# Performance work log

Hardware: AMD Instinct MI355X
Metric: run time of the kernel (lower is better)

Reference implementation:

```python
import jax, jax.numpy as jnp
import numpy as np

N, D, V, T = 2048, 64, 32000, 512
K_WTA = 256
X_DECAY, U_DECAY = 0.97, 0.97
SPIKE_RATE = 0.01
FORGET_ETA = 0.01
HOMEO_TAU = 1.0
GAMMA_MAX = 1.0


def ln_row(z, eps=1e-6):
    # torch .std is unbiased (ddof=1)
    m = z.mean(-1, keepdims=True)
    s = z.std(-1, ddof=1, keepdims=True)
    return (z - m) / (s + eps)


def setup_inputs() -> dict:
    key = jax.random.key(0)
    ks = jax.random.split(key, 6)
    return {
        "tokens": jax.random.randint(ks[0], (T,), 0, V),
        "spike_u": jax.random.uniform(ks[1], (T, N), dtype=jnp.float32),
        "E": jax.random.normal(ks[2], (D, N), dtype=jnp.float32) / np.sqrt(N).astype(np.float32),
        "Dx": jax.random.normal(ks[3], (N, D), dtype=jnp.float32) / np.sqrt(D).astype(np.float32),
        "Dy": jax.random.normal(ks[4], (N, D), dtype=jnp.float32) / np.sqrt(D).astype(np.float32),
        "token_emb": jax.random.normal(ks[5], (V, D), dtype=jnp.float32) / np.sqrt(D).astype(np.float32),
    }


def reference(tokens, spike_u, E, Dx, Dy, token_emb):
    def step(carry, inp):
        x, rho = carry
        tok, u = inp
        v_prev = token_emb[tok]                                   # (D,)
        x_t = X_DECAY * x + jax.nn.relu(Dx @ v_prev)              # (N,)
        x_t = x_t / (jnp.sum(jnp.abs(x_t)) + 1e-6)                # L1 normalize
        a_hat = ln_row(rho @ x_t)                                 # (D,) ln_before_Dy
        # branches=4 with elementwise softplus == softplus on full matvec
        y_core = jax.nn.softplus(Dy @ a_hat)                      # (N,)
        y_core = y_core + (u < SPIKE_RATE).astype(y_core.dtype)   # spike noise
        # k-WTA: keep top K_WTA entries
        _, idx = jax.lax.top_k(y_core, K_WTA)
        mask = jnp.zeros((N,), bool).at[idx].set(True)
        y_core = y_core * mask.astype(y_core.dtype)
        y_t = jax.nn.relu(y_core) * jax.nn.relu(x_t)
        # homeostasis (torch uses .item() -> constant scale)
        s = y_t.sum()
        scale = jnp.where(s > 1e-8, jnp.minimum(1.0, HOMEO_TAU / (s + 1e-8)), 1.0)
        y_t = y_t * jax.lax.stop_gradient(scale)
        v_star = ln_row(E @ y_t)                                  # (D,)
        # surprisal gain (torch uses .item() -> constant)
        p = jax.nn.softmax(v_star)
        H = -(p * jnp.log(p + 1e-12)).sum()
        gain = jnp.minimum(GAMMA_MAX, H / jnp.log(jnp.float32(D) + 1e-6) * GAMMA_MAX)
        gain = jax.lax.stop_gradient(gain)
        # dynamic top-k on x_t via rank masking (jit-safe data-dependent k)
        k_dyn = jnp.clip((N * (0.05 + 0.25 * gain)).astype(jnp.int32), 1, N)
        order = jnp.argsort(-x_t)
        ranks = jnp.zeros((N,), jnp.int32).at[order].set(jnp.arange(N, dtype=jnp.int32))
        x_t = x_t * (ranks < k_dyn).astype(x_t.dtype)
        # local forgetting on inactive columns, then Hebbian update
        inactive = (x_t <= 0).astype(rho.dtype)
        rho = rho * (1.0 - FORGET_ETA * inactive[None, :])
        rho = U_DECAY * (rho + gain * jnp.outer(v_prev, x_t))
        return (x_t, rho), v_star

    init = (jnp.zeros((N,), jnp.float32), jnp.zeros((D, N), jnp.float32))
    (_, _), v_stack = jax.lax.scan(step, init, (tokens, spike_u))
    return v_stack  # (T, D)
```

## Files before the change

kernel.cpp:

```cpp
#include <hip/hip_runtime.h>
#include <math.h>

#define NB   16
#define NTH  256
#define CH   128
#define NN   2048
#define DD   64
#define TT   512
#define KWTA 256
#define PA   65
#define PB   132

struct __align__(128) BarFlag { unsigned v; unsigned pad[31]; };
__device__ BarFlag g_flag[NB];
__device__ __align__(16) float  g_rf[NB][DD];
__device__ __align__(16) double g_L1[NB];
__device__ __align__(16) float  g_xg[NN];
__device__ __align__(16) float  g_yg[NN];
__device__ __align__(16) float  g_ET[NN*DD];

__global__ void bdh_init(const float* __restrict__ E) {
  const int gid = blockIdx.x * NTH + threadIdx.x;
  if (gid < NB) g_flag[gid].v = 0u;
  for (int idx = gid; idx < NN * DD; idx += 64 * NTH) {
    const int n = idx >> 6, d = idx & 63;
    g_ET[idx] = E[(size_t)d * NN + n];
  }
}

__device__ __forceinline__ void grid_barrier(unsigned& epoch) {
  epoch += 1u;
  __syncthreads();
  if (threadIdx.x < 64) {
    if (threadIdx.x == 0) {
      __threadfence();
      __hip_atomic_store(&g_flag[blockIdx.x].v, epoch, __ATOMIC_RELAXED,
                         __HIP_MEMORY_SCOPE_AGENT);
    }
    const int i = (int)threadIdx.x;
    for (;;) {
      const bool ok = (i >= NB) ||
        (__hip_atomic_load(&g_flag[i].v, __ATOMIC_RELAXED,
                           __HIP_MEMORY_SCOPE_AGENT) >= epoch);
      if (__all(ok)) break;
      __builtin_amdgcn_s_sleep(1);
    }
    __builtin_amdgcn_fence(__ATOMIC_ACQUIRE, "agent");
  }
  __syncthreads();
}

__device__ __forceinline__ double wredd(double v) {
  #pragma unroll
  for (int off = 32; off > 0; off >>= 1) v += __shfl_xor(v, off, 64);
  return v;
}
__device__ __forceinline__ float wredf(float v) {
  #pragma unroll
  for (int off = 32; off > 0; off >>= 1) v += __shfl_xor(v, off, 64);
  return v;
}

__device__ __forceinline__ unsigned select_mask(const unsigned* __restrict__ keys,
                                                int K, int tid,
                                                unsigned* __restrict__ hist,
                                                unsigned* __restrict__ hist2,
                                                unsigned* __restrict__ cw)
{
  const int wv = tid >> 6, lane = tid & 63;
  const int sub = tid & 7;
  uint4* H4 = (uint4*)hist;
  const uint4 z4 = {0u, 0u, 0u, 0u};
  unsigned prefix = 0u, pmask = 0u;
  int remK = K;
  #pragma unroll
  for (int lev = 0; lev < 4; ++lev) {
    const int shf = 24 - 8 * lev;
    #pragma unroll
    for (int j = 0; j < 8; ++j)
      if ((keys[j] & pmask) == prefix)
        atomicAdd(&hist[(((keys[j] >> shf) & 255u) << 3) + sub], 1u);
    __syncthreads();
    {
      const uint4 a = H4[tid * 2], bq = H4[tid * 2 + 1];
      hist2[tid] = a.x + a.y + a.z + a.w + bq.x + bq.y + bq.z + bq.w;
      H4[tid * 2] = z4;
      H4[tid * 2 + 1] = z4;
    }
    __syncthreads();
    const uint4 cc = ((const uint4*)hist2)[lane];
    unsigned c[4] = {cc.x, cc.y, cc.z, cc.w};
    unsigned s[4];
    s[3] = c[3]; s[2] = c[2] + s[3]; s[1] = c[1] + s[2]; s[0] = c[0] + s[1];
    unsigned SS = s[0];
    #pragma unroll
    for (int off = 1; off < 64; off <<= 1) {
      const unsigned o = __shfl_down(SS, off, 64);
      if (lane + off < 64) SS += o;
    }
    const unsigned T = SS - s[0];
    unsigned pk = 0u;
    #pragma unroll
    for (int k = 0; k < 4; ++k) {
      const unsigned A = s[k] + T;
      if (A >= (unsigned)remK && (A - c[k]) < (unsigned)remK)
        pk = (((unsigned)(4 * lane + k)) << 16) | (unsigned)(remK - (int)(A - c[k]));
    }
    const unsigned long long bal = __ballot(pk != 0u);
    const int src = __ffsll((long long)bal) - 1;
    pk = __shfl(pk, src, 64);
    prefix |= (pk >> 16) << shf;
    remK = (int)(pk & 0xffffu);
    pmask |= 255u << shf;
  }
  const unsigned thr = prefix;
  const unsigned R = (unsigned)remK;
  unsigned lc[8], cnt = 0u;
  #pragma unroll
  for (int j = 0; j < 8; ++j) { lc[j] = cnt; cnt += (keys[j] == thr) ? 1u : 0u; }
  unsigned e = cnt;
  #pragma unroll
  for (int off = 1; off < 64; off <<= 1) {
    const unsigned o = __shfl_up(e, off, 64);
    if (lane >= off) e += o;
  }
  if (lane == 63) cw[wv] = e;
  __syncthreads();
  unsigned base = 0u;
  for (int w = 0; w < wv; ++w) base += cw[w];
  const unsigned excl = base + e - cnt;
  unsigned mask = 0u;
  #pragma unroll
  for (int j = 0; j < 8; ++j)
    if (keys[j] > thr || (keys[j] == thr && excl + lc[j] < R)) mask |= 1u << j;
  return mask;
}

__global__ void __launch_bounds__(NTH)
bdh_main(const int* __restrict__ tokens, const float* __restrict__ spike_u,
         const float* __restrict__ Emat, const float* __restrict__ Dx,
         const float* __restrict__ Dy, const float* __restrict__ temb,
         float* __restrict__ out)
{
  __shared__ float sh_rho[DD][PB];
  __shared__ float sh_Dx[CH][PA];
  __shared__ float sh_Dy[CH][PA];
  __shared__ int   sh_tok[TT];
  __shared__ float sh_v[2][DD];
  __shared__ float sh_xstate[CH];
  __shared__ float sh_xtun[CH];
  __shared__ float sh_ahat[DD];
  __shared__ float sh_ffac[CH];
  __shared__ unsigned sh_hist[256*8];
  __shared__ unsigned sh_hist2[256];
  __shared__ unsigned sh_cw[8];
  __shared__ float sh_fmisc[4];
  __shared__ double sh_dred[8];
  __shared__ double sh_rd[4][DD];
  __shared__ float sh_gred[4][DD];
  __shared__ int   sh_aidx[KWTA];
  __shared__ float sh_aw[KWTA];

  const int tid  = threadIdx.x;
  const int b    = blockIdx.x;
  const int n0   = b * CH;
  const int i2   = tid >> 1;
  const int p2   = tid & 1;
  const int d4   = tid >> 2;
  const int p4   = tid & 3;
  const int lane = tid & 63;
  const int wv   = tid >> 6;
  unsigned epoch = 0u;

  for (int k = tid; k < TT; k += NTH) sh_tok[k] = tokens[k];
  for (int k = tid; k < DD*PB; k += NTH) (&sh_rho[0][0])[k] = 0.0f;
  for (int k = tid; k < 256*8; k += NTH) sh_hist[k] = 0u;
  if (tid < CH) sh_xstate[tid] = 0.0f;
  for (int r = wv; r < CH; r += 4) {
    sh_Dx[r][lane] = Dx[(size_t)(n0 + r)*DD + lane];
    sh_Dy[r][lane] = Dy[(size_t)(n0 + r)*DD + lane];
  }
  __syncthreads();
  if (tid < DD) sh_v[0][tid] = temb[(size_t)sh_tok[0]*DD + tid];
  __syncthreads();

  for (int t = 0; t < TT; ++t) {
    const int par = t & 1;

    float spu = 0.0f;
    if (p2 == 0) spu = spike_u[(size_t)t*NN + n0 + i2];
    if (t + 1 < TT && tid < DD)
      sh_v[par ^ 1][tid] = temb[(size_t)sh_tok[t + 1]*DD + tid];

    float d1 = 0.0f;
    {
      const float* dxr = &sh_Dx[i2][p2*32];
      const float* vv  = &sh_v[par][p2*32];
      #pragma unroll
      for (int j = 0; j < 32; ++j) d1 += dxr[j] * vv[j];
    }
    d1 += __shfl_xor(d1, 1, 64);
    float xnew = 0.0f;
    if (p2 == 0) {
      xnew = 0.97f * sh_xstate[i2] + fmaxf(d1, 0.0f);
      sh_xtun[i2] = xnew;
    }
    {
      double v = (p2 == 0) ? (double)fabsf(xnew) : 0.0;
      v = wredd(v);
      if (lane == 0) sh_dred[wv] = v;
      __syncthreads();
      if (tid == 0) g_L1[b] = sh_dred[0] + sh_dred[1] + sh_dred[2] + sh_dred[3];
    }
    float qa = 0.0f;
    {
      const float* rr = &sh_rho[d4][0];
      #pragma unroll
      for (int j = 0; j < 32; ++j) { const int c = p4 + 4*j; qa += rr[c] * sh_xtun[c]; }
    }
    qa += __shfl_xor(qa, 1, 64);
    qa += __shfl_xor(qa, 2, 64);
    if (p4 == 0) g_rf[b][d4] = qa;
    grid_barrier(epoch);

    {
      double acc = 0.0;
      #pragma unroll
      for (int j = 0; j < 4; ++j) acc += (double)g_rf[(wv<<2) + j][lane];
      sh_rd[wv][lane] = acc;
    }
    if (tid < 64) {
      double v = (tid < NB) ? g_L1[tid] : 0.0;
      v = wredd(v);
      if (tid == 0) sh_dred[0] = v;
    }
    __syncthreads();
    const float Lden = (float)sh_dred[0] + 1e-6f;
    if (tid < 64) {
      const double qd = sh_rd[0][tid] + sh_rd[1][tid] + sh_rd[2][tid] + sh_rd[3][tid];
      const float rf = (float)qd / Lden;
      const float m  = wredf(rf) * (1.0f/64.0f);
      const float dv = rf - m;
      const float sd = sqrtf(wredf(dv*dv) * (1.0f/63.0f));
      sh_ahat[tid] = dv / (sd + 1e-6f);
    } else if (tid < 192) {
      const int l = tid - 64;
      g_xg[n0 + l] = sh_xtun[l] / Lden;
    }
    __syncthreads();
    float d2 = 0.0f;
    {
      const float* dyr = &sh_Dy[i2][p2*32];
      const float* aa  = &sh_ahat[p2*32];
      #pragma unroll
      for (int j = 0; j < 32; ++j) d2 += dyr[j] * aa[j];
    }
    d2 += __shfl_xor(d2, 1, 64);
    if (p2 == 0) {
      const float sp = fmaxf(d2, 0.0f) + log1pf(expf(-fabsf(d2)));
      g_yg[n0 + i2] = sp + ((spu < 0.01f) ? 1.0f : 0.0f);
    }
    grid_barrier(epoch);

    unsigned ykeys[8], xkeys[8];
    {
      const float4* py = ((const float4*)g_yg) + tid*2;
      const float4* px = ((const float4*)g_xg) + tid*2;
      const float4 y0 = py[0], y1 = py[1];
      const float4 x0 = px[0], x1 = px[1];
      ykeys[0]=__float_as_uint(y0.x); ykeys[1]=__float_as_uint(y0.y);
      ykeys[2]=__float_as_uint(y0.z); ykeys[3]=__float_as_uint(y0.w);
      ykeys[4]=__float_as_uint(y1.x); ykeys[5]=__float_as_uint(y1.y);
      ykeys[6]=__float_as_uint(y1.z); ykeys[7]=__float_as_uint(y1.w);
      xkeys[0]=__float_as_uint(x0.x); xkeys[1]=__float_as_uint(x0.y);
      xkeys[2]=__float_as_uint(x0.z); xkeys[3]=__float_as_uint(x0.w);
      xkeys[4]=__float_as_uint(x1.x); xkeys[5]=__float_as_uint(x1.y);
      xkeys[6]=__float_as_uint(x1.z); xkeys[7]=__float_as_uint(x1.w);
    }
    const unsigned km = select_mask(ykeys, KWTA, tid, sh_hist, sh_hist2, sh_cw);
    float p[8]; unsigned nzm = 0u;
    #pragma unroll
    for (int j = 0; j < 8; ++j) {
      const float yv = __uint_as_float(ykeys[j]);
      const float xv = __uint_as_float(xkeys[j]);
      p[j] = yv * xv;
      if (((km >> j) & 1u) && xv > 0.0f) nzm |= 1u << j;
    }
    const unsigned cnt = (unsigned)__popc(nzm);
    {
      double sp = 0.0;
      #pragma unroll
      for (int j = 0; j < 8; ++j) if ((nzm >> j) & 1u) sp += (double)p[j];
      sp = wredd(sp);
      if (lane == 0) sh_dred[wv] = sp;
    }
    unsigned e = cnt;
    #pragma unroll
    for (int off = 1; off < 64; off <<= 1) {
      const unsigned o = __shfl_up(e, off, 64);
      if (lane >= off) e += o;
    }
    if (lane == 63) sh_cw[4 + wv] = e;
    __syncthreads();
    const float sf = (float)(sh_dred[0] + sh_dred[1] + sh_dred[2] + sh_dred[3]);
    const float scale = (sf > 1e-8f) ? fminf(1.0f, 1.0f/(sf + 1e-8f)) : 1.0f;
    const int m = (int)(sh_cw[4] + sh_cw[5] + sh_cw[6] + sh_cw[7]);
    {
      unsigned base = 0u;
      for (int w = 0; w < wv; ++w) base += sh_cw[4 + w];
      int pos = (int)(base + e - cnt);
      #pragma unroll
      for (int j = 0; j < 8; ++j)
        if ((nzm >> j) & 1u) { sh_aidx[pos] = 8*tid + j; sh_aw[pos] = scale * p[j]; ++pos; }
    }
    __syncthreads();
    {
      float a0 = 0.0f, a1 = 0.0f, a2 = 0.0f, a3 = 0.0f;
      int i = wv;
      for (; i + 12 < m; i += 16) {
        a0 = fmaf(sh_aw[i],      g_ET[(size_t)sh_aidx[i]     *DD + lane], a0);
        a1 = fmaf(sh_aw[i + 4],  g_ET[(size_t)sh_aidx[i + 4] *DD + lane], a1);
        a2 = fmaf(sh_aw[i + 8],  g_ET[(size_t)sh_aidx[i + 8] *DD + lane], a2);
        a3 = fmaf(sh_aw[i + 12], g_ET[(size_t)sh_aidx[i + 12]*DD + lane], a3);
      }
      for (; i < m; i += 4)
        a0 = fmaf(sh_aw[i], g_ET[(size_t)sh_aidx[i]*DD + lane], a0);
      sh_gred[wv][lane] = (a0 + a1) + (a2 + a3);
    }
    __syncthreads();
    if (tid < 64) {
      const float z = sh_gred[0][tid] + sh_gred[1][tid] + sh_gred[2][tid] + sh_gred[3][tid];
      const float mn = wredf(z) * (1.0f/64.0f);
      const float dv = z - mn;
      const float sd = sqrtf(wredf(dv*dv) * (1.0f/63.0f));
      const float vs = dv / (sd + 1e-6f);
      if (b == 0) out[t*DD + tid] = vs;
      float mx = vs;
      #pragma unroll
      for (int off = 32; off > 0; off >>= 1) mx = fmaxf(mx, __shfl_xor(mx, off, 64));
      const float ex = expf(vs - mx);
      const float se = wredf(ex);
      const float pp = ex / se;
      const float ht = wredf(-pp * logf(pp + 1e-12f));
      if (tid == 0) sh_fmisc[0] = fminf(1.0f, ht / logf(64.0f));
    }
    __syncthreads();
    const float gain = sh_fmisc[0];
    int kd = (int)(2048.0f * (0.05f + 0.25f * gain));
    kd = kd < 1 ? 1 : (kd > NN ? NN : kd);
    const unsigned xm = select_mask(xkeys, kd, tid, sh_hist, sh_hist2, sh_cw);
    #pragma unroll
    for (int j = 0; j < 8; ++j) {
      const int g = 8*tid + j;
      const unsigned l = (unsigned)(g - n0);
      if (l < (unsigned)CH) {
        const float xv = __uint_as_float(xkeys[j]);
        const float v = ((xm >> j) & 1u) ? xv : 0.0f;
        sh_xstate[l] = v;
        sh_ffac[l] = (v <= 0.0f) ? (1.0f - 0.01f) : 1.0f;
      }
    }
    __syncthreads();
    {
      const float vd = sh_v[par][d4];
      float* rr = &sh_rho[d4][0];
      #pragma unroll
      for (int j = 0; j < 32; ++j) {
        const int c = p4 + 4*j;
        rr[c] = 0.97f * (rr[c]*sh_ffac[c] + gain * (vd * sh_xstate[c]));
      }
    }
    __syncthreads();
  }
}

extern "C" void kernel_launch(void* const* d_in, const int* in_sizes, int n_in,
                              void* d_out, int out_size, void* d_ws, size_t ws_size,
                              hipStream_t stream) {
  const int*   tokens = (const int*)d_in[0];
  const float* spike  = (const float*)d_in[1];
  const float* Emat   = (const float*)d_in[2];
  const float* Dx     = (const float*)d_in[3];
  const float* Dy     = (const float*)d_in[4];
  const float* temb   = (const float*)d_in[5];
  float* out = (float*)d_out;
  (void)in_sizes; (void)n_in; (void)out_size; (void)d_ws; (void)ws_size;
  bdh_init<<<dim3(64), dim3(NTH), 0, stream>>>(Emat);
  bdh_main<<<dim3(NB), dim3(NTH), 0, stream>>>(tokens, spike, Emat, Dx, Dy, temb, out);
}
```

Before: 9.981 ms.

## Switch top-k selection to 12/12/8-bit radix passes and split grid barrier

Measured after the change: 10.07 ms. Within noise of the previous version (+0.9%).

```diff
diff --git a/kernel.cpp b/kernel.cpp
--- a/kernel.cpp
+++ b/kernel.cpp
@@ -28,15 +28,17 @@
   }
 }
 
-__device__ __forceinline__ void grid_barrier(unsigned& epoch) {
+__device__ __forceinline__ void bar_arrive(unsigned& epoch) {
   epoch += 1u;
   __syncthreads();
+  if (threadIdx.x == 0) {
+    __threadfence();
+    __hip_atomic_store(&g_flag[blockIdx.x].v, epoch, __ATOMIC_RELAXED,
+                       __HIP_MEMORY_SCOPE_AGENT);
+  }
+}
+__device__ __forceinline__ void bar_wait(unsigned epoch) {
   if (threadIdx.x < 64) {
-    if (threadIdx.x == 0) {
-      __threadfence();
-      __hip_atomic_store(&g_flag[blockIdx.x].v, epoch, __ATOMIC_RELAXED,
-                         __HIP_MEMORY_SCOPE_AGENT);
-    }
     const int i = (int)threadIdx.x;
     for (;;) {
       const bool ok = (i >= NB) ||
@@ -61,60 +63,85 @@
   return v;
 }
 
-__device__ __forceinline__ unsigned select_mask(const unsigned* __restrict__ keys,
-                                                int K, int tid,
-                                                unsigned* __restrict__ hist,
-                                                unsigned* __restrict__ hist2,
-                                                unsigned* __restrict__ cw)
-{
+__device__ __forceinline__ uint2 scan4096(const unsigned* __restrict__ h,
+                                          unsigned* __restrict__ coarse,
+                                          int tid, int lane, unsigned remK) {
+  const uint4* H4 = (const uint4*)h;
+  unsigned tot = 0u;
+  #pragma unroll
+  for (int k = 0; k < 4; ++k) {
+    const uint4 q = H4[tid * 4 + k];
+    tot += q.x + q.y + q.z + q.w;
+  }
+  coarse[tid] = tot;
+  __syncthreads();
+  const uint4 C = ((const uint4*)coarse)[lane];
+  const unsigned s3 = C.w, s2 = C.z + s3, s1 = C.y + s2, s0 = C.x + s1;
+  unsigned SS = s0;
+  #pragma unroll
+  for (int off = 1; off < 64; off <<= 1) {
+    const unsigned o = __shfl_down(SS, off, 64);
+    if (lane + off < 64) SS += o;
+  }
+  const unsigned T = SS - s0;
+  const unsigned cs[4] = {C.x, C.y, C.z, C.w};
+  const unsigned sf[4] = {s0, s1, s2, s3};
+  unsigned pk = 0u;
+  #pragma unroll
+  for (int k = 0; k < 4; ++k) {
+    const unsigned A = sf[k] + T;
+    if (A >= remK && A - cs[k] < remK)
+      pk = (((unsigned)(4 * lane + k)) << 16) | (remK - (A - cs[k]));
+  }
+  const unsigned long long bal = __ballot(pk != 0u);
+  const int src = __ffsll((long long)bal) - 1;
+  pk = __shfl(pk, src, 64);
+  const int tc = (int)(pk >> 16);
+  const unsigned rk = pk & 0xffffu;
+  const uint4 f0 = H4[tc*4+0], f1 = H4[tc*4+1], f2 = H4[tc*4+2], f3 = H4[tc*4+3];
+  const unsigned f[16] = {f0.x,f0.y,f0.z,f0.w, f1.x,f1.y,f1.z,f1.w,
+                          f2.x,f2.y,f2.z,f2.w, f3.x,f3.y,f3.z,f3.w};
+  unsigned FS[16];
+  FS[15] = f[15];
+  #pragma unroll
+  for (int k = 14; k >= 0; --k) FS[k] = f[k] + FS[k + 1];
+  unsigned bin = 0u, rem = rk;
+  #pragma unroll
+  for (int k = 0; k < 16; ++k)
+    if (FS[k] >= rk && FS[k] - f[k] < rk) { bin = (unsigned)(16*tc + k); rem = rk - (FS[k] - f[k]); }
+  return make_uint2(bin, rem);
+}
+
+__device__ __forceinline__ uint2 scan256(const unsigned* __restrict__ h,
+                                         int lane, unsigned remK) {
+  const uint4 C = ((const uint4*)h)[lane];
+  const unsigned s3 = C.w, s2 = C.z + s3, s1 = C.y + s2, s0 = C.x + s1;
+  unsigned SS = s0;
+  #pragma unroll
+  for (int off = 1; off < 64; off <<= 1) {
+    const unsigned o = __shfl_down(SS, off, 64);
+    if (lane + off < 64) SS += o;
+  }
+  const unsigned T = SS - s0;
+  const unsigned cs[4] = {C.x, C.y, C.z, C.w};
+  const unsigned sf[4] = {s0, s1, s2, s3};
+  unsigned pk = 0u;
+  #pragma unroll
+  for (int k = 0; k < 4; ++k) {
+    const unsigned A = sf[k] + T;
+    if (A >= remK && A - cs[k] < remK)
+      pk = (((unsigned)(4 * lane + k)) << 16) | (remK - (A - cs[k]));
+  }
+  const unsigned long long bal = __ballot(pk != 0u);
+  const int src = __ffsll((long long)bal) - 1;
+  pk = __shfl(pk, src, 64);
+  return make_uint2(pk >> 16, pk & 0xffffu);
+}
+
+__device__ __forceinline__ unsigned tie_mask(const unsigned* __restrict__ keys,
+                                             unsigned thr, unsigned R, int tid,
+                                             unsigned* __restrict__ cw) {
   const int wv = tid >> 6, lane = tid & 63;
-  const int sub = tid & 7;
-  uint4* H4 = (uint4*)hist;
-  const uint4 z4 = {0u, 0u, 0u, 0u};
-  unsigned prefix = 0u, pmask = 0u;
-  int remK = K;
-  #pragma unroll
-  for (int lev = 0; lev < 4; ++lev) {
-    const int shf = 24 - 8 * lev;
-    #pragma unroll
-    for (int j = 0; j < 8; ++j)
-      if ((keys[j] & pmask) == prefix)
-        atomicAdd(&hist[(((keys[j] >> shf) & 255u) << 3) + sub], 1u);
-    __syncthreads();
-    {
-      const uint4 a = H4[tid * 2], bq = H4[tid * 2 + 1];
-      hist2[tid] = a.x + a.y + a.z + a.w + bq.x + bq.y + bq.z + bq.w;
-      H4[tid * 2] = z4;
-      H4[tid * 2 + 1] = z4;
-    }
-    __syncthreads();
-    const uint4 cc = ((const uint4*)hist2)[lane];
-    unsigned c[4] = {cc.x, cc.y, cc.z, cc.w};
-    unsigned s[4];
-    s[3] = c[3]; s[2] = c[2] + s[3]; s[1] = c[1] + s[2]; s[0] = c[0] + s[1];
-    unsigned SS = s[0];
-    #pragma unroll
-    for (int off = 1; off < 64; off <<= 1) {
-      const unsigned o = __shfl_down(SS, off, 64);
-      if (lane + off < 64) SS += o;
-    }
-    const unsigned T = SS - s[0];
-    unsigned pk = 0u;
-    #pragma unroll
-    for (int k = 0; k < 4; ++k) {
-      const unsigned A = s[k] + T;
-      if (A >= (unsigned)remK && (A - c[k]) < (unsigned)remK)
-        pk = (((unsigned)(4 * lane + k)) << 16) | (unsigned)(remK - (int)(A - c[k]));
-    }
-    const unsigned long long bal = __ballot(pk != 0u);
-    const int src = __ffsll((long long)bal) - 1;
-    pk = __shfl(pk, src, 64);
-    prefix |= (pk >> 16) << shf;
-    remK = (int)(pk & 0xffffu);
-    pmask |= 255u << shf;
-  }
-  const unsigned thr = prefix;
-  const unsigned R = (unsigned)remK;
   unsigned lc[8], cnt = 0u;
   #pragma unroll
   for (int j = 0; j < 8; ++j) { lc[j] = cnt; cnt += (keys[j] == thr) ? 1u : 0u; }
@@ -151,8 +178,10 @@
   __shared__ float sh_xtun[CH];
   __shared__ float sh_ahat[DD];
   __shared__ float sh_ffac[CH];
-  __shared__ unsigned sh_hist[256*8];
-  __shared__ unsigned sh_hist2[256];
+  __shared__ __align__(16) unsigned sh_h1x[4096];
+  __shared__ __align__(16) unsigned sh_h1y[4096];
+  __shared__ __align__(16) unsigned sh_h3[256];
+  __shared__ __align__(16) unsigned sh_coarse[256];
   __shared__ unsigned sh_cw[8];
   __shared__ float sh_fmisc[4];
   __shared__ double sh_dred[8];
@@ -171,10 +200,16 @@
   const int lane = tid & 63;
   const int wv   = tid >> 6;
   unsigned epoch = 0u;
+  const uint4 z4 = {0u, 0u, 0u, 0u};
 
   for (int k = tid; k < TT; k += NTH) sh_tok[k] = tokens[k];
   for (int k = tid; k < DD*PB; k += NTH) (&sh_rho[0][0])[k] = 0.0f;
-  for (int k = tid; k < 256*8; k += NTH) sh_hist[k] = 0u;
+  {
+    uint4* Zx = (uint4*)sh_h1x; uint4* Zy = (uint4*)sh_h1y;
+    #pragma unroll
+    for (int k = 0; k < 4; ++k) { Zx[tid*4+k] = z4; Zy[tid*4+k] = z4; }
+    if (tid < 64) ((uint4*)sh_h3)[tid] = z4;
+  }
   if (tid < CH) sh_xstate[tid] = 0.0f;
   for (int r = wv; r < CH; r += 4) {
     sh_Dx[r][lane] = Dx[(size_t)(n0 + r)*DD + lane];
@@ -204,6 +239,7 @@
     if (p2 == 0) {
       xnew = 0.97f * sh_xstate[i2] + fmaxf(d1, 0.0f);
       sh_xtun[i2] = xnew;
+      g_xg[n0 + i2] = xnew;
     }
     {
       double v = (p2 == 0) ? (double)fabsf(xnew) : 0.0;
@@ -221,8 +257,11 @@
     qa += __shfl_xor(qa, 1, 64);
     qa += __shfl_xor(qa, 2, 64);
     if (p4 == 0) g_rf[b][d4] = qa;
-    grid_barrier(epoch);
-
+    bar_arrive(epoch);
+    bar_wait(epoch);
+
+    const float4* pxu = ((const float4*)g_xg) + tid*2;
+    const float4 xu0 = pxu[0], xu1 = pxu[1];
     {
       double acc = 0.0;
       #pragma unroll
@@ -239,13 +278,16 @@
     if (tid < 64) {
       const double qd = sh_rd[0][tid] + sh_rd[1][tid] + sh_rd[2][tid] + sh_rd[3][tid];
       const float rf = (float)qd / Lden;
-      const float m  = wredf(rf) * (1.0f/64.0f);
-      const float dv = rf - m;
+      const float mm = wredf(rf) * (1.0f/64.0f);
+      const float dv = rf - mm;
       const float sd = sqrtf(wredf(dv*dv) * (1.0f/63.0f));
       sh_ahat[tid] = dv / (sd + 1e-6f);
-    } else if (tid < 192) {
-      const int l = tid - 64;
-      g_xg[n0 + l] = sh_xtun[l] / Lden;
+    }
+    unsigned xkeys[8];
+    {
+      const float xf[8] = {xu0.x,xu0.y,xu0.z,xu0.w, xu1.x,xu1.y,xu1.z,xu1.w};
+      #pragma unroll
+      for (int j = 0; j < 8; ++j) xkeys[j] = __float_as_uint(xf[j] / Lden);
     }
     __syncthreads();
     float d2 = 0.0f;
@@ -260,24 +302,52 @@
       const float sp = fmaxf(d2, 0.0f) + log1pf(expf(-fabsf(d2)));
       g_yg[n0 + i2] = sp + ((spu < 0.01f) ? 1.0f : 0.0f);
     }
-    grid_barrier(epoch);
-
-    unsigned ykeys[8], xkeys[8];
+    bar_arrive(epoch);
+    #pragma unroll
+    for (int j = 0; j < 8; ++j) atomicAdd(&sh_h1x[xkeys[j] >> 20], 1u);
+    bar_wait(epoch);
+
+    unsigned ykeys[8];
     {
       const float4* py = ((const float4*)g_yg) + tid*2;
-      const float4* px = ((const float4*)g_xg) + tid*2;
       const float4 y0 = py[0], y1 = py[1];
-      const float4 x0 = px[0], x1 = px[1];
       ykeys[0]=__float_as_uint(y0.x); ykeys[1]=__float_as_uint(y0.y);
       ykeys[2]=__float_as_uint(y0.z); ykeys[3]=__float_as_uint(y0.w);
       ykeys[4]=__float_as_uint(y1.x); ykeys[5]=__float_as_uint(y1.y);
       ykeys[6]=__float_as_uint(y1.z); ykeys[7]=__float_as_uint(y1.w);
-      xkeys[0]=__float_as_uint(x0.x); xkeys[1]=__float_as_uint(x0.y);
-      xkeys[2]=__float_as_uint(x0.z); xkeys[3]=__float_as_uint(x0.w);
-      xkeys[4]=__float_as_uint(x1.x); xkeys[5]=__float_as_uint(x1.y);
-      xkeys[6]=__float_as_uint(x1.z); xkeys[7]=__float_as_uint(x1.w);
-    }
-    const unsigned km = select_mask(ykeys, KWTA, tid, sh_hist, sh_hist2, sh_cw);
+    }
+    #pragma unroll
+    for (int j = 0; j < 8; ++j) atomicAdd(&sh_h1y[ykeys[j] >> 20], 1u);
+    __syncthreads();
+    const uint2 yr1 = scan4096(sh_h1y, sh_coarse, tid, lane, KWTA);
+    __syncthreads();
+    {
+      uint4* Z = (uint4*)sh_h1y;
+      #pragma unroll
+      for (int k = 0; k < 4; ++k) Z[tid*4+k] = z4;
+    }
+    __syncthreads();
+    #pragma unroll
+    for (int j = 0; j < 8; ++j)
+      if ((ykeys[j] >> 20) == yr1.x)
+        atomicAdd(&sh_h1y[(ykeys[j] >> 8) & 4095u], 1u);
+    __syncthreads();
+    const uint2 yr2 = scan4096(sh_h1y, sh_coarse, tid, lane, yr1.y);
+    const unsigned ypre = (yr1.x << 12) | yr2.x;
+    #pragma unroll
+    for (int j = 0; j < 8; ++j)
+      if ((ykeys[j] >> 8) == ypre)
+        atomicAdd(&sh_h3[ykeys[j] & 255u], 1u);
+    __syncthreads();
+    const uint2 yr3 = scan256(sh_h3, lane, yr2.y);
+    const unsigned thrY = (ypre << 8) | yr3.x;
+    const unsigned km = tie_mask(ykeys, thrY, yr3.y, tid, sh_cw);
+    {
+      uint4* Z = (uint4*)sh_h1y;
+      #pragma unroll
+      for (int k = 0; k < 4; ++k) Z[tid*4+k] = z4;
+      if (tid < 64) ((uint4*)sh_h3)[tid] = z4;
+    }
     float p[8]; unsigned nzm = 0u;
     #pragma unroll
     for (int j = 0; j < 8; ++j) {
@@ -346,9 +416,35 @@
     }
     __syncthreads();
     const float gain = sh_fmisc[0];
-    int kd = (int)(2048.0f * (0.05f + 0.25f * gain));
-    kd = kd < 1 ? 1 : (kd > NN ? NN : kd);
-    const unsigned xm = select_mask(xkeys, kd, tid, sh_hist, sh_hist2, sh_cw);
+    int kdi = (int)(2048.0f * (0.05f + 0.25f * gain));
+    kdi = kdi < 1 ? 1 : (kdi > NN ? NN : kdi);
+    const uint2 xr1 = scan4096(sh_h1x, sh_coarse, tid, lane, (unsigned)kdi);
+    #pragma unroll
+    for (int j = 0; j < 8; ++j)
+      if ((xkeys[j] >> 20) == xr1.x)
+        atomicAdd(&sh_h1y[(xkeys[j] >> 8) & 4095u], 1u);
+    __syncthreads();
+    {
+      uint4* Z = (uint4*)sh_h1x;
+      #pragma unroll
+      for (int k = 0; k < 4; ++k) Z[tid*4+k] = z4;
+    }
+    const uint2 xr2 = scan4096(sh_h1y, sh_coarse, tid, lane, xr1.y);
+    const unsigned xpre = (xr1.x << 12) | xr2.x;
+    #pragma unroll
+    for (int j = 0; j < 8; ++j)
+      if ((xkeys[j] >> 8) == xpre)
+        atomicAdd(&sh_h3[xkeys[j] & 255u], 1u);
+    __syncthreads();
+    {
+      uint4* Z = (uint4*)sh_h1y;
+      #pragma unroll
+      for (int k = 0; k < 4; ++k) Z[tid*4+k] = z4;
+    }
+    const uint2 xr3 = scan256(sh_h3, lane, xr2.y);
+    const unsigned thrX = (xpre << 8) | xr3.x;
+    const unsigned xm = tie_mask(xkeys, thrX, xr3.y, tid, sh_cw);
+    if (tid < 64) ((uint4*)sh_h3)[tid] = z4;
     #pragma unroll
     for (int j = 0; j < 8; ++j) {
       const int g = 8*tid + j;
```

## Use cache-bypassing stores/loads to drop barrier fences and early-publish x

Applied to the files above, without the earlier changes.

Result: faster. 9.760 ms (-2.2%).

```diff
diff --git a/kernel.cpp b/kernel.cpp
--- a/kernel.cpp
+++ b/kernel.cpp
@@ -11,6 +11,8 @@
 #define PA   65
 #define PB   132
 
+typedef float f32x4 __attribute__((ext_vector_type(4)));
+
 struct __align__(128) BarFlag { unsigned v; unsigned pad[31]; };
 __device__ BarFlag g_flag[NB];
 __device__ __align__(16) float  g_rf[NB][DD];
@@ -28,15 +30,23 @@
   }
 }
 
-__device__ __forceinline__ void grid_barrier(unsigned& epoch) {
+__device__ __forceinline__ void st_coh_f32(float* p, float v) {
+  asm volatile("global_store_dword %0, %1, off sc0 sc1" :: "v"(p), "v"(v) : "memory");
+}
+__device__ __forceinline__ void st_coh_f64(double* p, double v) {
+  asm volatile("global_store_dwordx2 %0, %1, off sc0 sc1" :: "v"(p), "v"(v) : "memory");
+}
+
+__device__ __forceinline__ void bar_arrive(unsigned& epoch) {
   epoch += 1u;
+  asm volatile("s_waitcnt vmcnt(0)" ::: "memory");
   __syncthreads();
+  if (threadIdx.x == 0)
+    __hip_atomic_store(&g_flag[blockIdx.x].v, epoch, __ATOMIC_RELAXED,
+                       __HIP_MEMORY_SCOPE_AGENT);
+}
+__device__ __forceinline__ void bar_wait(unsigned epoch) {
   if (threadIdx.x < 64) {
-    if (threadIdx.x == 0) {
-      __threadfence();
-      __hip_atomic_store(&g_flag[blockIdx.x].v, epoch, __ATOMIC_RELAXED,
-                         __HIP_MEMORY_SCOPE_AGENT);
-    }
     const int i = (int)threadIdx.x;
     for (;;) {
       const bool ok = (i >= NB) ||
@@ -45,7 +55,6 @@
       if (__all(ok)) break;
       __builtin_amdgcn_s_sleep(1);
     }
-    __builtin_amdgcn_fence(__ATOMIC_ACQUIRE, "agent");
   }
   __syncthreads();
 }
@@ -204,13 +213,15 @@
     if (p2 == 0) {
       xnew = 0.97f * sh_xstate[i2] + fmaxf(d1, 0.0f);
       sh_xtun[i2] = xnew;
+      st_coh_f32(&g_xg[n0 + i2], xnew);
     }
     {
       double v = (p2 == 0) ? (double)fabsf(xnew) : 0.0;
       v = wredd(v);
       if (lane == 0) sh_dred[wv] = v;
       __syncthreads();
-      if (tid == 0) g_L1[b] = sh_dred[0] + sh_dred[1] + sh_dred[2] + sh_dred[3];
+      if (tid == 0) st_coh_f64(&g_L1[b],
+                               sh_dred[0] + sh_dred[1] + sh_dred[2] + sh_dred[3]);
     }
     float qa = 0.0f;
     {
@@ -220,18 +231,40 @@
     }
     qa += __shfl_xor(qa, 1, 64);
     qa += __shfl_xor(qa, 2, 64);
-    if (p4 == 0) g_rf[b][d4] = qa;
-    grid_barrier(epoch);
-
+    if (p4 == 0) st_coh_f32(&g_rf[b][d4], qa);
+    bar_arrive(epoch);
+    bar_wait(epoch);
+
+    f32x4 xu0, xu1; float rf0, rf1, rf2, rf3;
+    {
+      const float* xp = g_xg + tid*8;
+      const float* rp = &g_rf[wv*4][lane];
+      asm volatile(
+        "global_load_dwordx4 %0, %6, off sc0 sc1\n\t"
+        "global_load_dwordx4 %1, %6, off offset:16 sc0 sc1\n\t"
+        "global_load_dword %2, %7, off sc0 sc1\n\t"
+        "global_load_dword %3, %7, off offset:256 sc0 sc1\n\t"
+        "global_load_dword %4, %7, off offset:512 sc0 sc1\n\t"
+        "global_load_dword %5, %7, off offset:768 sc0 sc1\n\t"
+        "s_waitcnt vmcnt(0)"
+        : "=&v"(xu0), "=&v"(xu1), "=&v"(rf0), "=&v"(rf1), "=&v"(rf2), "=&v"(rf3)
+        : "v"(xp), "v"(rp)
+        : "memory");
+      __builtin_amdgcn_sched_barrier(0);
+    }
     {
       double acc = 0.0;
-      #pragma unroll
-      for (int j = 0; j < 4; ++j) acc += (double)g_rf[(wv<<2) + j][lane];
+      acc += (double)rf0; acc += (double)rf1; acc += (double)rf2; acc += (double)rf3;
       sh_rd[wv][lane] = acc;
     }
     if (tid < 64) {
-      double v = (tid < NB) ? g_L1[tid] : 0.0;
-      v = wredd(v);
+      double lv = 0.0;
+      if (tid < NB) {
+        asm volatile("global_load_dwordx2 %0, %1, off sc0 sc1\n\ts_waitcnt vmcnt(0)"
+                     : "=&v"(lv) : "v"(&g_L1[tid]) : "memory");
+      }
+      __builtin_amdgcn_sched_barrier(0);
+      const double v = wredd(lv);
       if (tid == 0) sh_dred[0] = v;
     }
     __syncthreads();
@@ -239,13 +272,16 @@
     if (tid < 64) {
       const double qd = sh_rd[0][tid] + sh_rd[1][tid] + sh_rd[2][tid] + sh_rd[3][tid];
       const float rf = (float)qd / Lden;
-      const float m  = wredf(rf) * (1.0f/64.0f);
-      const float dv = rf - m;
+      const float mm = wredf(rf) * (1.0f/64.0f);
+      const float dv = rf - mm;
       const float sd = sqrtf(wredf(dv*dv) * (1.0f/63.0f));
       sh_ahat[tid] = dv / (sd + 1e-6f);
-    } else if (tid < 192) {
-      const int l = tid - 64;
-      g_xg[n0 + l] = sh_xtun[l] / Lden;
+    }
+    unsigned xkeys[8];
+    {
+      const float xf[8] = {xu0[0],xu0[1],xu0[2],xu0[3], xu1[0],xu1[1],xu1[2],xu1[3]};
+      #pragma unroll
+      for (int j = 0; j < 8; ++j) xkeys[j] = __float_as_uint(xf[j] / Lden);
     }
     __syncthreads();
     float d2 = 0.0f;
@@ -258,24 +294,25 @@
     d2 += __shfl_xor(d2, 1, 64);
     if (p2 == 0) {
       const float sp = fmaxf(d2, 0.0f) + log1pf(expf(-fabsf(d2)));
-      g_yg[n0 + i2] = sp + ((spu < 0.01f) ? 1.0f : 0.0f);
-    }
-    grid_barrier(epoch);
-
-    unsigned ykeys[8], xkeys[8];
-    {
-      const float4* py = ((const float4*)g_yg) + tid*2;
-      const float4* px = ((const float4*)g_xg) + tid*2;
-      const float4 y0 = py[0], y1 = py[1];
-      const float4 x0 = px[0], x1 = px[1];
-      ykeys[0]=__float_as_uint(y0.x); ykeys[1]=__float_as_uint(y0.y);
-      ykeys[2]=__float_as_uint(y0.z); ykeys[3]=__float_as_uint(y0.w);
-      ykeys[4]=__float_as_uint(y1.x); ykeys[5]=__float_as_uint(y1.y);
-      ykeys[6]=__float_as_uint(y1.z); ykeys[7]=__float_as_uint(y1.w);
-      xkeys[0]=__float_as_uint(x0.x); xkeys[1]=__float_as_uint(x0.y);
-      xkeys[2]=__float_as_uint(x0.z); xkeys[3]=__float_as_uint(x0.w);
-      xkeys[4]=__float_as_uint(x1.x); xkeys[5]=__float_as_uint(x1.y);
-      xkeys[6]=__float_as_uint(x1.z); xkeys[7]=__float_as_uint(x1.w);
+      st_coh_f32(&g_yg[n0 + i2], sp + ((spu < 0.01f) ? 1.0f : 0.0f));
+    }
+    bar_arrive(epoch);
+    bar_wait(epoch);
+
+    unsigned ykeys[8];
+    {
+      f32x4 yv0, yv1;
+      const float* yp = g_yg + tid*8;
+      asm volatile(
+        "global_load_dwordx4 %0, %2, off sc0 sc1\n\t"
+        "global_load_dwordx4 %1, %2, off offset:16 sc0 sc1\n\t"
+        "s_waitcnt vmcnt(0)"
+        : "=&v"(yv0), "=&v"(yv1) : "v"(yp) : "memory");
+      __builtin_amdgcn_sched_barrier(0);
+      ykeys[0]=__float_as_uint(yv0[0]); ykeys[1]=__float_as_uint(yv0[1]);
+      ykeys[2]=__float_as_uint(yv0[2]); ykeys[3]=__float_as_uint(yv0[3]);
+      ykeys[4]=__float_as_uint(yv1[0]); ykeys[5]=__float_as_uint(yv1[1]);
+      ykeys[6]=__float_as_uint(yv1[2]); ykeys[7]=__float_as_uint(yv1[3]);
     }
     const unsigned km = select_mask(ykeys, KWTA, tid, sh_hist, sh_hist2, sh_cw);
     float p[8]; unsigned nzm = 0u;
@@ -346,9 +383,9 @@
     }
     __syncthreads();
     const float gain = sh_fmisc[0];
-    int kd = (int)(2048.0f * (0.05f + 0.25f * gain));
-    kd = kd < 1 ? 1 : (kd > NN ? NN : kd);
-    const unsigned xm = select_mask(xkeys, kd, tid, sh_hist, sh_hist2, sh_cw);
+    int kdi = (int)(2048.0f * (0.05f + 0.25f * gain));
+    kdi = kdi < 1 ? 1 : (kdi > NN ? NN : kdi);
+    const unsigned xm = select_mask(xkeys, kdi, tid, sh_hist, sh_hist2, sh_cw);
     #pragma unroll
     for (int j = 0; j < 8; ++j) {
       const int g = 8*tid + j;
```

## Replace grid barriers with tagged value-flag pairs polled by consumers

Applied to the files above, without the earlier changes.

After: 12.74 ms. 1.28x slower.

```diff
diff --git a/kernel.cpp b/kernel.cpp
--- a/kernel.cpp
+++ b/kernel.cpp
@@ -11,43 +11,32 @@
 #define PA   65
 #define PB   132
 
-struct __align__(128) BarFlag { unsigned v; unsigned pad[31]; };
-__device__ BarFlag g_flag[NB];
-__device__ __align__(16) float  g_rf[NB][DD];
-__device__ __align__(16) double g_L1[NB];
-__device__ __align__(16) float  g_xg[NN];
-__device__ __align__(16) float  g_yg[NN];
-__device__ __align__(16) float  g_ET[NN*DD];
+typedef unsigned long long u64;
+
+__device__ __align__(16) u64 g_xp[2][NN];
+__device__ __align__(16) u64 g_rp[2][NB][DD];
+__device__ __align__(16) u64 g_lp[2][NB][2];
+__device__ __align__(16) u64 g_yp[2][NN];
+__device__ __align__(16) float g_ET[NN*DD];
 
 __global__ void bdh_init(const float* __restrict__ E) {
   const int gid = blockIdx.x * NTH + threadIdx.x;
-  if (gid < NB) g_flag[gid].v = 0u;
-  for (int idx = gid; idx < NN * DD; idx += 64 * NTH) {
+  const int nthread = 64 * NTH;
+  for (int k = gid; k < 2*NN; k += nthread) { ((u64*)g_xp)[k] = 0ull; ((u64*)g_yp)[k] = 0ull; }
+  for (int k = gid; k < 2*NB*DD; k += nthread) ((u64*)g_rp)[k] = 0ull;
+  if (gid < 2*NB*2) ((u64*)g_lp)[gid] = 0ull;
+  for (int idx = gid; idx < NN * DD; idx += nthread) {
     const int n = idx >> 6, d = idx & 63;
     g_ET[idx] = E[(size_t)d * NN + n];
   }
 }
 
-__device__ __forceinline__ void grid_barrier(unsigned& epoch) {
-  epoch += 1u;
-  __syncthreads();
-  if (threadIdx.x < 64) {
-    if (threadIdx.x == 0) {
-      __threadfence();
-      __hip_atomic_store(&g_flag[blockIdx.x].v, epoch, __ATOMIC_RELAXED,
-                         __HIP_MEMORY_SCOPE_AGENT);
-    }
-    const int i = (int)threadIdx.x;
-    for (;;) {
-      const bool ok = (i >= NB) ||
-        (__hip_atomic_load(&g_flag[i].v, __ATOMIC_RELAXED,
-                           __HIP_MEMORY_SCOPE_AGENT) >= epoch);
-      if (__all(ok)) break;
-      __builtin_amdgcn_s_sleep(1);
-    }
-    __builtin_amdgcn_fence(__ATOMIC_ACQUIRE, "agent");
-  }
-  __syncthreads();
+__device__ __forceinline__ void st_pair(u64* p, unsigned valbits, unsigned tag) {
+  __hip_atomic_store(p, ((u64)tag << 32) | (u64)valbits,
+                     __ATOMIC_RELAXED, __HIP_MEMORY_SCOPE_AGENT);
+}
+__device__ __forceinline__ u64 ld_pair(const u64* p) {
+  return __hip_atomic_load(p, __ATOMIC_RELAXED, __HIP_MEMORY_SCOPE_AGENT);
 }
 
 __device__ __forceinline__ double wredd(double v) {
@@ -59,6 +48,19 @@
   #pragma unroll
   for (int off = 32; off > 0; off >>= 1) v += __shfl_xor(v, off, 64);
   return v;
+}
+
+__device__ __forceinline__ void poll8(const u64* __restrict__ p, unsigned want,
+                                      unsigned* __restrict__ outb) {
+  unsigned got = 0u;
+  while (got != 0xffu) {
+    #pragma unroll
+    for (int j = 0; j < 8; ++j)
+      if (!((got >> j) & 1u)) {
+        const u64 w = ld_pair(&p[j]);
+        if ((unsigned)(w >> 32) == want) { outb[j] = (unsigned)w; got |= 1u << j; }
+      }
+  }
 }
 
 __device__ __forceinline__ unsigned select_mask(const unsigned* __restrict__ keys,
@@ -156,7 +158,6 @@
   __shared__ unsigned sh_cw[8];
   __shared__ float sh_fmisc[4];
   __shared__ double sh_dred[8];
-  __shared__ double sh_rd[4][DD];
   __shared__ float sh_gred[4][DD];
   __shared__ int   sh_aidx[KWTA];
   __shared__ float sh_aw[KWTA];
@@ -170,7 +171,6 @@
   const int p4   = tid & 3;
   const int lane = tid & 63;
   const int wv   = tid >> 6;
-  unsigned epoch = 0u;
 
   for (int k = tid; k < TT; k += NTH) sh_tok[k] = tokens[k];
   for (int k = tid; k < DD*PB; k += NTH) (&sh_rho[0][0])[k] = 0.0f;
@@ -186,6 +186,7 @@
 
   for (int t = 0; t < TT; ++t) {
     const int par = t & 1;
+    const unsigned want = (unsigned)(t + 1);
 
     float spu = 0.0f;
     if (p2 == 0) spu = spike_u[(size_t)t*NN + n0 + i2];
@@ -204,13 +205,19 @@
     if (p2 == 0) {
       xnew = 0.97f * sh_xstate[i2] + fmaxf(d1, 0.0f);
       sh_xtun[i2] = xnew;
+      st_pair(&g_xp[par][n0 + i2], __float_as_uint(xnew), want);
     }
     {
       double v = (p2 == 0) ? (double)fabsf(xnew) : 0.0;
       v = wredd(v);
       if (lane == 0) sh_dred[wv] = v;
       __syncthreads();
-      if (tid == 0) g_L1[b] = sh_dred[0] + sh_dred[1] + sh_dred[2] + sh_dred[3];
+      if (tid == 0) {
+        const double L = sh_dred[0] + sh_dred[1] + sh_dred[2] + sh_dred[3];
+        const u64 lb = __double_as_longlong(L);
+        st_pair(&g_lp[par][b][0], (unsigned)lb, want);
+        st_pair(&g_lp[par][b][1], (unsigned)(lb >> 32), want);
+      }
     }
     float qa = 0.0f;
     {
@@ -220,32 +227,53 @@
     }
     qa += __shfl_xor(qa, 1, 64);
     qa += __shfl_xor(qa, 2, 64);
-    if (p4 == 0) g_rf[b][d4] = qa;
-    grid_barrier(epoch);
-
-    {
-      double acc = 0.0;
-      #pragma unroll
-      for (int j = 0; j < 4; ++j) acc += (double)g_rf[(wv<<2) + j][lane];
-      sh_rd[wv][lane] = acc;
-    }
-    if (tid < 64) {
-      double v = (tid < NB) ? g_L1[tid] : 0.0;
-      v = wredd(v);
-      if (tid == 0) sh_dred[0] = v;
-    }
-    __syncthreads();
-    const float Lden = (float)sh_dred[0] + 1e-6f;
-    if (tid < 64) {
-      const double qd = sh_rd[0][tid] + sh_rd[1][tid] + sh_rd[2][tid] + sh_rd[3][tid];
+    if (p4 == 0) st_pair(&g_rp[par][b][d4], __float_as_uint(qa), want);
+
+    double lv = 0.0;
+    if (lane < 16) {
+      unsigned got = 0u, lo = 0u, hi = 0u;
+      while (got != 3u) {
+        if (!(got & 1u)) { const u64 w = ld_pair(&g_lp[par][lane][0]);
+          if ((unsigned)(w >> 32) == want) { lo = (unsigned)w; got |= 1u; } }
+        if (!(got & 2u)) { const u64 w = ld_pair(&g_lp[par][lane][1]);
+          if ((unsigned)(w >> 32) == want) { hi = (unsigned)w; got |= 2u; } }
+      }
+      lv = __longlong_as_double(((u64)hi << 32) | (u64)lo);
+    }
+    const double L1tot = wredd(lv);
+    const float Lden = (float)L1tot + 1e-6f;
+    unsigned xub[8];
+    poll8(&g_xp[par][tid*8], want, xub);
+    unsigned xkeys[8];
+    #pragma unroll
+    for (int j = 0; j < 8; ++j)
+      xkeys[j] = __float_as_uint(__uint_as_float(xub[j]) / Lden);
+    if (wv == 0) {
+      float rv[16];
+      unsigned got = 0u;
+      while (got != 0xffffu) {
+        #pragma unroll
+        for (int bb = 0; bb < 16; ++bb)
+          if (!((got >> bb) & 1u)) {
+            const u64 w = ld_pair(&g_rp[par][bb][lane]);
+            if ((unsigned)(w >> 32) == want) { rv[bb] = __uint_as_float((unsigned)w); got |= 1u << bb; }
+          }
+      }
+      double a0 = 0.0, a1 = 0.0, a2 = 0.0, a3 = 0.0;
+      #pragma unroll
+      for (int j = 0; j < 4; ++j) a0 += (double)rv[j];
+      #pragma unroll
+      for (int j = 4; j < 8; ++j) a1 += (double)rv[j];
+      #pragma unroll
+      for (int j = 8; j < 12; ++j) a2 += (double)rv[j];
+      #pragma unroll
+      for (int j = 12; j < 16; ++j) a3 += (double)rv[j];
+      const double qd = ((a0 + a1) + a2) + a3;
       const float rf = (float)qd / Lden;
-      const float m  = wredf(rf) * (1.0f/64.0f);
-      const float dv = rf - m;
+      const float mm = wredf(rf) * (1.0f/64.0f);
+      const float dv = rf - mm;
       const float sd = sqrtf(wredf(dv*dv) * (1.0f/63.0f));
-      sh_ahat[tid] = dv / (sd + 1e-6f);
-    } else if (tid < 192) {
-      const int l = tid - 64;
-      g_xg[n0 + l] = sh_xtun[l] / Lden;
+      sh_ahat[lane] = dv / (sd + 1e-6f);
     }
     __syncthreads();
     float d2 = 0.0f;
@@ -258,25 +286,12 @@
     d2 += __shfl_xor(d2, 1, 64);
     if (p2 == 0) {
       const float sp = fmaxf(d2, 0.0f) + log1pf(expf(-fabsf(d2)));
-      g_yg[n0 + i2] = sp + ((spu < 0.01f) ? 1.0f : 0.0f);
-    }
-    grid_barrier(epoch);
-
-    unsigned ykeys[8], xkeys[8];
-    {
-      const float4* py = ((const float4*)g_yg) + tid*2;
-      const float4* px = ((const float4*)g_xg) + tid*2;
-      const float4 y0 = py[0], y1 = py[1];
-      const float4 x0 = px[0], x1 = px[1];
-      ykeys[0]=__float_as_uint(y0.x); ykeys[1]=__float_as_uint(y0.y);
-      ykeys[2]=__float_as_uint(y0.z); ykeys[3]=__float_as_uint(y0.w);
-      ykeys[4]=__float_as_uint(y1.x); ykeys[5]=__float_as_uint(y1.y);
-      ykeys[6]=__float_as_uint(y1.z); ykeys[7]=__float_as_uint(y1.w);
-      xkeys[0]=__float_as_uint(x0.x); xkeys[1]=__float_as_uint(x0.y);
-      xkeys[2]=__float_as_uint(x0.z); xkeys[3]=__float_as_uint(x0.w);
-      xkeys[4]=__float_as_uint(x1.x); xkeys[5]=__float_as_uint(x1.y);
-      xkeys[6]=__float_as_uint(x1.z); xkeys[7]=__float_as_uint(x1.w);
-    }
+      st_pair(&g_yp[par][n0 + i2],
+              __float_as_uint(sp + ((spu < 0.01f) ? 1.0f : 0.0f)), want);
+    }
+
+    unsigned ykeys[8];
+    poll8(&g_yp[par][tid*8], want, ykeys);
     const unsigned km = select_mask(ykeys, KWTA, tid, sh_hist, sh_hist2, sh_cw);
     float p[8]; unsigned nzm = 0u;
     #pragma unroll
@@ -346,9 +361,9 @@
     }
     __syncthreads();
     const float gain = sh_fmisc[0];
-    int kd = (int)(2048.0f * (0.05f + 0.25f * gain));
-    kd = kd < 1 ? 1 : (kd > NN ? NN : kd);
-    const unsigned xm = select_mask(xkeys, kd, tid, sh_hist, sh_hist2, sh_cw);
+    int kdi = (int)(2048.0f * (0.05f + 0.25f * gain));
+    kdi = kdi < 1 ? 1 : (kdi > NN ? NN : kdi);
+    const unsigned xm = select_mask(xkeys, kdi, tid, sh_hist, sh_hist2, sh_cw);
     #pragma unroll
     for (int j = 0; j < 8; ++j) {
       const int g = 8*tid + j;
```
